# Performance work log

Measured on AMD Instinct MI355X. Metric: run time of the kernel, lower is better.

Reference implementation:

```python
import jax, jax.numpy as jnp
import numpy as np

TOP_K = 2  # config.n_expert_per_token


def setup_inputs() -> dict:
    key = jax.random.key(0)
    ks = jax.random.split(key, 5)
    B, T, C, E, F = 2, 2048, 2048, 8, 1024
    scale = 0.02
    return {
        "x": jax.random.normal(ks[0], (B, T, C), jnp.float32),
        "w_router": jax.random.normal(ks[1], (C, E), jnp.float32) * scale,
        "w1": jax.random.normal(ks[2], (E, C, F), jnp.float32) * scale,  # fc_1 (gate proj)
        "w3": jax.random.normal(ks[3], (E, C, F), jnp.float32) * scale,  # fc_2 (up proj)
        "w2": jax.random.normal(ks[4], (E, F, C), jnp.float32) * scale,  # proj (down)
    }


def reference(x, w_router, w1, w3, w2):
    B, T, C = x.shape
    xt = x.reshape(-1, C)                                  # [N, C]
    N = xt.shape[0]
    E = w_router.shape[1]
    # Router: topk logits, softmax over the selected k in fp32
    logits = xt @ w_router                                 # [N, E]
    top_vals, top_idx = jax.lax.top_k(logits, TOP_K)       # [N, k]
    probs = jax.nn.softmax(top_vals.astype(jnp.float32), axis=1).astype(xt.dtype)
    # Per-token per-expert combine weight (0 for unselected experts).
    # topk indices are distinct per token, so scatter-add == scatter-set.
    w = jnp.zeros((N, E), xt.dtype).at[jnp.arange(N)[:, None], top_idx].add(probs)  # [N, E]
    # Dense grouped SwiGLU expert MLPs; zero-weight tokens contribute nothing.
    g = jnp.einsum('nc,ecf->enf', xt, w1)                  # [E, N, F]
    u = jnp.einsum('nc,ecf->enf', xt, w3)                  # [E, N, F]
    h = jax.nn.silu(g) * u                                 # [E, N, F]
    outs = jnp.einsum('enf,efc->enc', h, w2)               # [E, N, C]
    y = jnp.einsum('enc,ne->nc', outs, w)                  # weighted combine
    return y.reshape(B, T, C)
```

## Files before the change

### kernel.cpp

```cpp
#include <hip/hip_runtime.h>
#include <hip/hip_bf16.h>
#include <stdint.h>

#define N_TOK 4096
#define CDIM 2048
#define EXP 8
#define FDIM 1024
#define LDSTRIDE 40

typedef __attribute__((ext_vector_type(4))) float f32x4;
typedef __attribute__((ext_vector_type(8))) short bf16x8;

__global__ __launch_bounds__(256) void transpose_to_bf16(
    const float* __restrict__ in, __hip_bfloat16* __restrict__ out, int R, int Cc) {
  __shared__ float tile[32][33];
  int e = blockIdx.z;
  const float* ip = in + (size_t)e * R * Cc;
  __hip_bfloat16* op = out + (size_t)e * R * Cc;
  int r0 = blockIdx.y * 32, c0 = blockIdx.x * 32;
  int tc = threadIdx.x & 31, tr = threadIdx.x >> 5;
#pragma unroll
  for (int i = 0; i < 4; i++) {
    int r = tr + i * 8;
    tile[r][tc] = ip[(size_t)(r0 + r) * Cc + c0 + tc];
  }
  __syncthreads();
#pragma unroll
  for (int i = 0; i < 4; i++) {
    int r = tr + i * 8;
    op[(size_t)(c0 + r) * R + r0 + tc] = __float2bfloat16(tile[tc][r]);
  }
}

__global__ __launch_bounds__(256) void router_kernel(
    const float* __restrict__ x, const float* __restrict__ wr,
    __hip_bfloat16* __restrict__ x_bf, int* __restrict__ counts,
    int* __restrict__ pair_expert, float* __restrict__ pair_prob) {
  int tok = blockIdx.x;
  const float* xr = x + (size_t)tok * CDIM;
  int t = threadIdx.x;
  float acc[EXP];
#pragma unroll
  for (int e = 0; e < EXP; e++) acc[e] = 0.f;
#pragma unroll
  for (int j = 0; j < 8; j++) {
    int c = j * 256 + t;
    float xv = xr[c];
    x_bf[(size_t)tok * CDIM + c] = __float2bfloat16(xv);
    const float4* wr4 = (const float4*)(wr + (size_t)c * EXP);
    float4 wa = wr4[0], wb = wr4[1];
    acc[0] += xv * wa.x; acc[1] += xv * wa.y; acc[2] += xv * wa.z; acc[3] += xv * wa.w;
    acc[4] += xv * wb.x; acc[5] += xv * wb.y; acc[6] += xv * wb.z; acc[7] += xv * wb.w;
  }
#pragma unroll
  for (int e = 0; e < EXP; e++) {
#pragma unroll
    for (int off = 32; off > 0; off >>= 1) acc[e] += __shfl_down(acc[e], off, 64);
  }
  __shared__ float wsum[4][EXP];
  int wid = t >> 6, lane = t & 63;
  if (lane == 0) {
#pragma unroll
    for (int e = 0; e < EXP; e++) wsum[wid][e] = acc[e];
  }
  __syncthreads();
  if (t == 0) {
    float lg[EXP];
#pragma unroll
    for (int e = 0; e < EXP; e++) lg[e] = wsum[0][e] + wsum[1][e] + wsum[2][e] + wsum[3][e];
    int i0 = 0;
#pragma unroll
    for (int e = 1; e < EXP; e++) if (lg[e] > lg[i0]) i0 = e;
    int i1 = (i0 == 0) ? 1 : 0;
#pragma unroll
    for (int e = 0; e < EXP; e++) if (e != i0 && lg[e] > lg[i1]) i1 = e;
    float e1 = __expf(lg[i1] - lg[i0]);
    float p0 = 1.f / (1.f + e1);
    pair_expert[tok * 2 + 0] = i0;
    pair_expert[tok * 2 + 1] = i1;
    pair_prob[tok * 2 + 0] = p0;
    pair_prob[tok * 2 + 1] = e1 * p0;
    atomicAdd(&counts[i0], 1);
    atomicAdd(&counts[i1], 1);
  }
}

__global__ void scan_kernel(const int* __restrict__ counts, int* __restrict__ bases) {
  if (threadIdx.x == 0) {
    int s = 0;
    for (int e = 0; e < EXP; e++) { bases[e] = s; s += counts[e]; }
  }
}

__global__ __launch_bounds__(256) void scatter_kernel(
    const int* __restrict__ pair_expert, const int* __restrict__ bases,
    int* __restrict__ cursors, int* __restrict__ lists) {
  int tok = blockIdx.x * 256 + threadIdx.x;
  if (tok >= N_TOK) return;
#pragma unroll
  for (int k = 0; k < 2; k++) {
    int e = pair_expert[tok * 2 + k];
    int pos = atomicAdd(&cursors[e], 1);
    lists[bases[e] + pos] = tok * 2 + k;
  }
}

__global__ __launch_bounds__(256) void gemm1_kernel(
    const __hip_bfloat16* __restrict__ xbf, const __hip_bfloat16* __restrict__ w1t,
    const __hip_bfloat16* __restrict__ w3t, const int* __restrict__ counts,
    const int* __restrict__ bases, const int* __restrict__ lists,
    __hip_bfloat16* __restrict__ h) {
  int e = blockIdx.z;
  int n_e = counts[e];
  int m0 = blockIdx.y * 128;
  if (m0 >= n_e) return;
  int base = bases[e];
  int f0 = blockIdx.x * 64;

  __shared__ short As[128 * LDSTRIDE];
  __shared__ short B1s[64 * LDSTRIDE];
  __shared__ short B3s[64 * LDSTRIDE];

  int t = threadIdx.x;
  int lane = t & 63, wid = t >> 6;
  int wm = (wid & 1) * 64, wf = (wid >> 1) * 32;

  int arow = t >> 1;
  int achunk = (t & 1) * 16;
  int rr = m0 + arow;
  int pair = lists[base + ((rr < n_e) ? rr : 0)];
  int tokA = pair >> 1;

  const short* xs = (const short*)xbf;
  const short* b1p = (const short*)(w1t) + (size_t)e * FDIM * CDIM;
  const short* b3p = (const short*)(w3t) + (size_t)e * FDIM * CDIM;
  int brow = (t & 127) >> 1;
  bool doB1 = (t < 128);
  const short* bsrc = doB1 ? b1p : b3p;
  short* bdst = doB1 ? B1s : B3s;

  f32x4 zero = {0.f, 0.f, 0.f, 0.f};
  f32x4 accg[4][2], accu[4][2];
#pragma unroll
  for (int i = 0; i < 4; i++)
#pragma unroll
    for (int j = 0; j < 2; j++) { accg[i][j] = zero; accu[i][j] = zero; }

  for (int kk = 0; kk < CDIM; kk += 32) {
    __syncthreads();
    {
      const int4* src = (const int4*)(xs + (size_t)tokA * CDIM + kk + achunk);
      int4* dst = (int4*)(As + arow * LDSTRIDE + achunk);
      dst[0] = src[0];
      dst[1] = src[1];
      const int4* src2 = (const int4*)(bsrc + (size_t)(f0 + brow) * CDIM + kk + achunk);
      int4* dst2 = (int4*)(bdst + brow * LDSTRIDE + achunk);
      dst2[0] = src2[0];
      dst2[1] = src2[1];
    }
    __syncthreads();
    int kq = (lane >> 4) * 8;
    int rsel = lane & 15;
    bf16x8 af[4], b1f[2], b3f[2];
#pragma unroll
    for (int i = 0; i < 4; i++)
      af[i] = *(const bf16x8*)(As + (wm + i * 16 + rsel) * LDSTRIDE + kq);
#pragma unroll
    for (int j = 0; j < 2; j++) {
      b1f[j] = *(const bf16x8*)(B1s + (wf + j * 16 + rsel) * LDSTRIDE + kq);
      b3f[j] = *(const bf16x8*)(B3s + (wf + j * 16 + rsel) * LDSTRIDE + kq);
    }
#pragma unroll
    for (int i = 0; i < 4; i++)
#pragma unroll
      for (int j = 0; j < 2; j++) {
        accg[i][j] = __builtin_amdgcn_mfma_f32_16x16x32_bf16(af[i], b1f[j], accg[i][j], 0, 0, 0);
        accu[i][j] = __builtin_amdgcn_mfma_f32_16x16x32_bf16(af[i], b3f[j], accu[i][j], 0, 0, 0);
      }
  }

  int col = lane & 15;
  int rbase = (lane >> 4) * 4;
#pragma unroll
  for (int i = 0; i < 4; i++) {
#pragma unroll
    for (int r = 0; r < 4; r++) {
      int m = m0 + wm + i * 16 + rbase + r;
      if (m < n_e) {
        size_t hrow = (size_t)(base + m) * FDIM;
#pragma unroll
        for (int j = 0; j < 2; j++) {
          int f = f0 + wf + j * 16 + col;
          float g = accg[i][j][r];
          float u = accu[i][j][r];
          float sg = g / (1.f + __expf(-g));
          h[hrow + f] = __float2bfloat16(sg * u);
        }
      }
    }
  }
}

__global__ __launch_bounds__(256) void gemm2_kernel(
    const __hip_bfloat16* __restrict__ h, const __hip_bfloat16* __restrict__ w2t,
    const int* __restrict__ counts, const int* __restrict__ bases,
    const int* __restrict__ lists, const float* __restrict__ pair_prob,
    float* __restrict__ out) {
  int e = blockIdx.z;
  int n_e = counts[e];
  int m0 = blockIdx.y * 128;
  if (m0 >= n_e) return;
  int base = bases[e];
  int c0 = blockIdx.x * 128;

  __shared__ short As[128 * LDSTRIDE];
  __shared__ short Bs[128 * LDSTRIDE];

  int t = threadIdx.x;
  int lane = t & 63, wid = t >> 6;
  int wm = (wid & 1) * 64, wn = (wid >> 1) * 64;

  int arow = t >> 1;
  int achunk = (t & 1) * 16;
  int hr = base + m0 + arow;
  if (hr > 2 * N_TOK - 1) hr = 2 * N_TOK - 1;
  const short* hp = (const short*)h;
  const short* bp = (const short*)(w2t) + (size_t)e * CDIM * FDIM;

  f32x4 zero = {0.f, 0.f, 0.f, 0.f};
  f32x4 acc[4][4];
#pragma unroll
  for (int i = 0; i < 4; i++)
#pragma unroll
    for (int j = 0; j < 4; j++) acc[i][j] = zero;

  for (int kk = 0; kk < FDIM; kk += 32) {
    __syncthreads();
    {
      const int4* src = (const int4*)(hp + (size_t)hr * FDIM + kk + achunk);
      int4* dst = (int4*)(As + arow * LDSTRIDE + achunk);
      dst[0] = src[0];
      dst[1] = src[1];
      const int4* src2 = (const int4*)(bp + (size_t)(c0 + arow) * FDIM + kk + achunk);
      int4* dst2 = (int4*)(Bs + arow * LDSTRIDE + achunk);
      dst2[0] = src2[0];
      dst2[1] = src2[1];
    }
    __syncthreads();
    int kq = (lane >> 4) * 8;
    int rsel = lane & 15;
    bf16x8 af[4], bfr[4];
#pragma unroll
    for (int i = 0; i < 4; i++)
      af[i] = *(const bf16x8*)(As + (wm + i * 16 + rsel) * LDSTRIDE + kq);
#pragma unroll
    for (int j = 0; j < 4; j++)
      bfr[j] = *(const bf16x8*)(Bs + (wn + j * 16 + rsel) * LDSTRIDE + kq);
#pragma unroll
    for (int i = 0; i < 4; i++)
#pragma unroll
      for (int j = 0; j < 4; j++)
        acc[i][j] = __builtin_amdgcn_mfma_f32_16x16x32_bf16(af[i], bfr[j], acc[i][j], 0, 0, 0);
  }

  int col = lane & 15;
  int rbase = (lane >> 4) * 4;
#pragma unroll
  for (int i = 0; i < 4; i++) {
#pragma unroll
    for (int r = 0; r < 4; r++) {
      int m = m0 + wm + i * 16 + rbase + r;
      if (m < n_e) {
        int pr = lists[base + m];
        int tok = pr >> 1;
        float p = pair_prob[pr];
        size_t orow = (size_t)tok * CDIM;
#pragma unroll
        for (int j = 0; j < 4; j++) {
          int c = c0 + wn + j * 16 + col;
          atomicAdd(&out[orow + c], acc[i][j][r] * p);
        }
      }
    }
  }
}

extern "C" void kernel_launch(void* const* d_in, const int* in_sizes, int n_in,
                              void* d_out, int out_size, void* d_ws, size_t ws_size,
                              hipStream_t stream) {
  const float* x  = (const float*)d_in[0];
  const float* wr = (const float*)d_in[1];
  const float* w1 = (const float*)d_in[2];
  const float* w3 = (const float*)d_in[3];
  const float* w2 = (const float*)d_in[4];
  float* out = (float*)d_out;

  char* ws = (char*)d_ws;
  __hip_bfloat16* x_bf = (__hip_bfloat16*)(ws);
  __hip_bfloat16* h    = (__hip_bfloat16*)(ws + 16777216);
  __hip_bfloat16* w1t  = (__hip_bfloat16*)(ws + 33554432);
  __hip_bfloat16* w3t  = (__hip_bfloat16*)(ws + 67108864);
  __hip_bfloat16* w2t  = (__hip_bfloat16*)(ws + 100663296);
  int* counts  = (int*)(ws + 134217728);
  int* bases   = counts + 8;
  int* cursors = counts + 16;
  int* pair_expert = (int*)(ws + 134217728 + 128);
  float* pair_prob = (float*)(ws + 134217728 + 128 + 32768);
  int* lists       = (int*)(ws + 134217728 + 128 + 65536);

  hipMemsetAsync(d_out, 0, (size_t)N_TOK * CDIM * sizeof(float), stream);
  hipMemsetAsync(counts, 0, 128, stream);

  transpose_to_bf16<<<dim3(FDIM / 32, CDIM / 32, EXP), 256, 0, stream>>>(w1, w1t, CDIM, FDIM);
  transpose_to_bf16<<<dim3(FDIM / 32, CDIM / 32, EXP), 256, 0, stream>>>(w3, w3t, CDIM, FDIM);
  transpose_to_bf16<<<dim3(CDIM / 32, FDIM / 32, EXP), 256, 0, stream>>>(w2, w2t, FDIM, CDIM);

  router_kernel<<<N_TOK, 256, 0, stream>>>(x, wr, x_bf, counts, pair_expert, pair_prob);
  scan_kernel<<<1, 64, 0, stream>>>(counts, bases);
  scatter_kernel<<<N_TOK / 256, 256, 0, stream>>>(pair_expert, bases, cursors, lists);

  gemm1_kernel<<<dim3(FDIM / 64, N_TOK / 128, EXP), 256, 0, stream>>>(
      x_bf, w1t, w3t, counts, bases, lists, h);
  gemm2_kernel<<<dim3(CDIM / 128, N_TOK / 128, EXP), 256, 0, stream>>>(
      h, w2t, counts, bases, lists, pair_prob, out);
}
```

Before: 632.2 us.

## Use direct global-to-LDS loads in expert GEMMs and vectorize weight transpose

Both expert GEMM kernels now stage A and B tiles with global_load_lds 16-byte transfers straight into LDS, which skips the register round trip. The LDS tiles are re-laid out into 16x32 fragment blocks so each lane reads its MFMA operand contiguously. The weight transpose kernel now uses float4 loads, 64-row tiles and 16-byte bf16 stores to cut transaction count. The new LDS layout has no padding, so fragment reads may hit bank conflicts, and the global reads per row become more scattered across lanes.

```diff
diff --git a/kernel.cpp b/kernel.cpp
--- a/kernel.cpp
+++ b/kernel.cpp
@@ -6,30 +6,40 @@
 #define CDIM 2048
 #define EXP 8
 #define FDIM 1024
-#define LDSTRIDE 40
 
 typedef __attribute__((ext_vector_type(4))) float f32x4;
 typedef __attribute__((ext_vector_type(8))) short bf16x8;
 
+__device__ __forceinline__ void g2l16(const void* g, void* l) {
+  __builtin_amdgcn_global_load_lds(
+      (const __attribute__((address_space(1))) void*)g,
+      (__attribute__((address_space(3))) void*)l, 16, 0, 0);
+}
+
 __global__ __launch_bounds__(256) void transpose_to_bf16(
     const float* __restrict__ in, __hip_bfloat16* __restrict__ out, int R, int Cc) {
-  __shared__ float tile[32][33];
+  __shared__ float tile[32][65];
   int e = blockIdx.z;
   const float* ip = in + (size_t)e * R * Cc;
   __hip_bfloat16* op = out + (size_t)e * R * Cc;
-  int r0 = blockIdx.y * 32, c0 = blockIdx.x * 32;
-  int tc = threadIdx.x & 31, tr = threadIdx.x >> 5;
-#pragma unroll
-  for (int i = 0; i < 4; i++) {
-    int r = tr + i * 8;
-    tile[r][tc] = ip[(size_t)(r0 + r) * Cc + c0 + tc];
+  int r0 = blockIdx.y * 64, c0 = blockIdx.x * 32;
+  int t = threadIdx.x;
+#pragma unroll
+  for (int p = 0; p < 2; p++) {
+    int f = t + p * 256;
+    int r = f >> 3, c4 = (f & 7) * 4;
+    float4 v = *(const float4*)(ip + (size_t)(r0 + r) * Cc + c0 + c4);
+    tile[c4 + 0][r] = v.x;
+    tile[c4 + 1][r] = v.y;
+    tile[c4 + 2][r] = v.z;
+    tile[c4 + 3][r] = v.w;
   }
   __syncthreads();
-#pragma unroll
-  for (int i = 0; i < 4; i++) {
-    int r = tr + i * 8;
-    op[(size_t)(c0 + r) * R + r0 + tc] = __float2bfloat16(tile[tc][r]);
-  }
+  int c = t >> 3, seg = (t & 7) * 8;
+  union { int4 v; __hip_bfloat16 h[8]; } u;
+#pragma unroll
+  for (int j = 0; j < 8; j++) u.h[j] = __float2bfloat16(tile[c][seg + j]);
+  *(int4*)(op + (size_t)(c0 + c) * R + r0 + seg) = u.v;
 }
 
 __global__ __launch_bounds__(256) void router_kernel(
@@ -117,27 +127,31 @@
   int base = bases[e];
   int f0 = blockIdx.x * 64;
 
-  __shared__ short As[128 * LDSTRIDE];
-  __shared__ short B1s[64 * LDSTRIDE];
-  __shared__ short B3s[64 * LDSTRIDE];
+  __shared__ alignas(16) short As[128 * 32];
+  __shared__ alignas(16) short B1s[64 * 32];
+  __shared__ alignas(16) short B3s[64 * 32];
 
   int t = threadIdx.x;
   int lane = t & 63, wid = t >> 6;
-  int wm = (wid & 1) * 64, wf = (wid >> 1) * 32;
-
-  int arow = t >> 1;
-  int achunk = (t & 1) * 16;
-  int rr = m0 + arow;
-  int pair = lists[base + ((rr < n_e) ? rr : 0)];
-  int tokA = pair >> 1;
+  int lr = lane & 15;
+  int lk = (lane >> 4) * 8;
 
   const short* xs = (const short*)xbf;
-  const short* b1p = (const short*)(w1t) + (size_t)e * FDIM * CDIM;
-  const short* b3p = (const short*)(w3t) + (size_t)e * FDIM * CDIM;
-  int brow = (t & 127) >> 1;
-  bool doB1 = (t < 128);
-  const short* bsrc = doB1 ? b1p : b3p;
-  short* bdst = doB1 ? B1s : B3s;
+  const short* b1p = (const short*)w1t + (size_t)e * FDIM * CDIM;
+  const short* b3p = (const short*)w3t + (size_t)e * FDIM * CDIM;
+
+  int r0a = m0 + (2 * wid) * 16 + lr;
+  int r1a = m0 + (2 * wid + 1) * 16 + lr;
+  int t0 = lists[base + ((r0a < n_e) ? r0a : (n_e - 1))] >> 1;
+  int t1 = lists[base + ((r1a < n_e) ? r1a : (n_e - 1))] >> 1;
+  const short* aptr0 = xs + (size_t)t0 * CDIM + lk;
+  const short* aptr1 = xs + (size_t)t1 * CDIM + lk;
+  const short* bptr1 = b1p + (size_t)(f0 + wid * 16 + lr) * CDIM + lk;
+  const short* bptr3 = b3p + (size_t)(f0 + wid * 16 + lr) * CDIM + lk;
+  short* ldsA0 = &As[(2 * wid) * 512];
+  short* ldsA1 = &As[(2 * wid + 1) * 512];
+  short* ldsB1 = &B1s[wid * 512];
+  short* ldsB3 = &B3s[wid * 512];
 
   f32x4 zero = {0.f, 0.f, 0.f, 0.f};
   f32x4 accg[4][2], accu[4][2];
@@ -146,29 +160,24 @@
 #pragma unroll
     for (int j = 0; j < 2; j++) { accg[i][j] = zero; accu[i][j] = zero; }
 
+  int asub = (wid & 1) * 4;
+  int bsub = (wid >> 1) * 2;
+
   for (int kk = 0; kk < CDIM; kk += 32) {
     __syncthreads();
-    {
-      const int4* src = (const int4*)(xs + (size_t)tokA * CDIM + kk + achunk);
-      int4* dst = (int4*)(As + arow * LDSTRIDE + achunk);
-      dst[0] = src[0];
-      dst[1] = src[1];
-      const int4* src2 = (const int4*)(bsrc + (size_t)(f0 + brow) * CDIM + kk + achunk);
-      int4* dst2 = (int4*)(bdst + brow * LDSTRIDE + achunk);
-      dst2[0] = src2[0];
-      dst2[1] = src2[1];
-    }
+    g2l16(aptr0 + kk, ldsA0);
+    g2l16(aptr1 + kk, ldsA1);
+    g2l16(bptr1 + kk, ldsB1);
+    g2l16(bptr3 + kk, ldsB3);
     __syncthreads();
-    int kq = (lane >> 4) * 8;
-    int rsel = lane & 15;
     bf16x8 af[4], b1f[2], b3f[2];
 #pragma unroll
     for (int i = 0; i < 4; i++)
-      af[i] = *(const bf16x8*)(As + (wm + i * 16 + rsel) * LDSTRIDE + kq);
+      af[i] = *(const bf16x8*)&As[(asub + i) * 512 + lane * 8];
 #pragma unroll
     for (int j = 0; j < 2; j++) {
-      b1f[j] = *(const bf16x8*)(B1s + (wf + j * 16 + rsel) * LDSTRIDE + kq);
-      b3f[j] = *(const bf16x8*)(B3s + (wf + j * 16 + rsel) * LDSTRIDE + kq);
+      b1f[j] = *(const bf16x8*)&B1s[(bsub + j) * 512 + lane * 8];
+      b3f[j] = *(const bf16x8*)&B3s[(bsub + j) * 512 + lane * 8];
     }
 #pragma unroll
     for (int i = 0; i < 4; i++)
@@ -179,6 +188,7 @@
       }
   }
 
+  int wm = (wid & 1) * 64, wf = (wid >> 1) * 32;
   int col = lane & 15;
   int rbase = (lane >> 4) * 4;
 #pragma unroll
@@ -213,19 +223,29 @@
   int base = bases[e];
   int c0 = blockIdx.x * 128;
 
-  __shared__ short As[128 * LDSTRIDE];
-  __shared__ short Bs[128 * LDSTRIDE];
+  __shared__ alignas(16) short As[128 * 32];
+  __shared__ alignas(16) short Bs[128 * 32];
 
   int t = threadIdx.x;
   int lane = t & 63, wid = t >> 6;
-  int wm = (wid & 1) * 64, wn = (wid >> 1) * 64;
-
-  int arow = t >> 1;
-  int achunk = (t & 1) * 16;
-  int hr = base + m0 + arow;
-  if (hr > 2 * N_TOK - 1) hr = 2 * N_TOK - 1;
+  int lr = lane & 15;
+  int lk = (lane >> 4) * 8;
+
   const short* hp = (const short*)h;
-  const short* bp = (const short*)(w2t) + (size_t)e * CDIM * FDIM;
+  const short* bp = (const short*)w2t + (size_t)e * CDIM * FDIM;
+
+  int hr0 = base + m0 + (2 * wid) * 16 + lr;
+  int hr1 = base + m0 + (2 * wid + 1) * 16 + lr;
+  if (hr0 > 2 * N_TOK - 1) hr0 = 2 * N_TOK - 1;
+  if (hr1 > 2 * N_TOK - 1) hr1 = 2 * N_TOK - 1;
+  const short* aptr0 = hp + (size_t)hr0 * FDIM + lk;
+  const short* aptr1 = hp + (size_t)hr1 * FDIM + lk;
+  const short* bptr0 = bp + (size_t)(c0 + (2 * wid) * 16 + lr) * FDIM + lk;
+  const short* bptr1 = bp + (size_t)(c0 + (2 * wid + 1) * 16 + lr) * FDIM + lk;
+  short* ldsA0 = &As[(2 * wid) * 512];
+  short* ldsA1 = &As[(2 * wid + 1) * 512];
+  short* ldsB0 = &Bs[(2 * wid) * 512];
+  short* ldsB1 = &Bs[(2 * wid + 1) * 512];
 
   f32x4 zero = {0.f, 0.f, 0.f, 0.f};
   f32x4 acc[4][4];
@@ -234,28 +254,23 @@
 #pragma unroll
     for (int j = 0; j < 4; j++) acc[i][j] = zero;
 
+  int asub = (wid & 1) * 4;
+  int bsub = (wid >> 1) * 4;
+
   for (int kk = 0; kk < FDIM; kk += 32) {
     __syncthreads();
-    {
-      const int4* src = (const int4*)(hp + (size_t)hr * FDIM + kk + achunk);
-      int4* dst = (int4*)(As + arow * LDSTRIDE + achunk);
-      dst[0] = src[0];
-      dst[1] = src[1];
-      const int4* src2 = (const int4*)(bp + (size_t)(c0 + arow) * FDIM + kk + achunk);
-      int4* dst2 = (int4*)(Bs + arow * LDSTRIDE + achunk);
-      dst2[0] = src2[0];
-      dst2[1] = src2[1];
-    }
+    g2l16(aptr0 + kk, ldsA0);
+    g2l16(aptr1 + kk, ldsA1);
+    g2l16(bptr0 + kk, ldsB0);
+    g2l16(bptr1 + kk, ldsB1);
     __syncthreads();
-    int kq = (lane >> 4) * 8;
-    int rsel = lane & 15;
     bf16x8 af[4], bfr[4];
 #pragma unroll
     for (int i = 0; i < 4; i++)
-      af[i] = *(const bf16x8*)(As + (wm + i * 16 + rsel) * LDSTRIDE + kq);
+      af[i] = *(const bf16x8*)&As[(asub + i) * 512 + lane * 8];
 #pragma unroll
     for (int j = 0; j < 4; j++)
-      bfr[j] = *(const bf16x8*)(Bs + (wn + j * 16 + rsel) * LDSTRIDE + kq);
+      bfr[j] = *(const bf16x8*)&Bs[(bsub + j) * 512 + lane * 8];
 #pragma unroll
     for (int i = 0; i < 4; i++)
 #pragma unroll
@@ -263,6 +278,7 @@
         acc[i][j] = __builtin_amdgcn_mfma_f32_16x16x32_bf16(af[i], bfr[j], acc[i][j], 0, 0, 0);
   }
 
+  int wm = (wid & 1) * 64, wn = (wid >> 1) * 64;
   int col = lane & 15;
   int rbase = (lane >> 4) * 4;
 #pragma unroll
@@ -311,9 +327,9 @@
   hipMemsetAsync(d_out, 0, (size_t)N_TOK * CDIM * sizeof(float), stream);
   hipMemsetAsync(counts, 0, 128, stream);
 
-  transpose_to_bf16<<<dim3(FDIM / 32, CDIM / 32, EXP), 256, 0, stream>>>(w1, w1t, CDIM, FDIM);
-  transpose_to_bf16<<<dim3(FDIM / 32, CDIM / 32, EXP), 256, 0, stream>>>(w3, w3t, CDIM, FDIM);
-  transpose_to_bf16<<<dim3(CDIM / 32, FDIM / 32, EXP), 256, 0, stream>>>(w2, w2t, FDIM, CDIM);
+  transpose_to_bf16<<<dim3(FDIM / 32, CDIM / 64, EXP), 256, 0, stream>>>(w1, w1t, CDIM, FDIM);
+  transpose_to_bf16<<<dim3(FDIM / 32, CDIM / 64, EXP), 256, 0, stream>>>(w3, w3t, CDIM, FDIM);
+  transpose_to_bf16<<<dim3(CDIM / 32, FDIM / 64, EXP), 256, 0, stream>>>(w2, w2t, FDIM, CDIM);
 
   router_kernel<<<N_TOK, 256, 0, stream>>>(x, wr, x_bf, counts, pair_expert, pair_prob);
   scan_kernel<<<1, 64, 0, stream>>>(counts, bases);
```

Result: slower. 688.6 us (+8.9%).

## Register-prefetch next K tile in MoE GEMMs and vectorize weight transpose

Applied to the files above, without the earlier changes.

Both grouped GEMM kernels now load the next K-slice from global memory into registers right after the barrier, so the fetch overlaps the MFMA work on the current LDS tile instead of stalling at the top of each iteration. The weight transpose-to-bf16 kernel moves to 64x64 tiles, reading with float4 and writing 16 bf16 values per thread as two int4 stores, which cuts the number of memory instructions. This costs extra live registers in the GEMMs, which may lower occupancy. The transpose's column-major LDS writes may also hit bank conflicts.

```diff
diff --git a/kernel.cpp b/kernel.cpp
--- a/kernel.cpp
+++ b/kernel.cpp
@@ -13,22 +13,33 @@
 
 __global__ __launch_bounds__(256) void transpose_to_bf16(
     const float* __restrict__ in, __hip_bfloat16* __restrict__ out, int R, int Cc) {
-  __shared__ float tile[32][33];
+  __shared__ float tile[64][65];
   int e = blockIdx.z;
   const float* ip = in + (size_t)e * R * Cc;
   __hip_bfloat16* op = out + (size_t)e * R * Cc;
-  int r0 = blockIdx.y * 32, c0 = blockIdx.x * 32;
-  int tc = threadIdx.x & 31, tr = threadIdx.x >> 5;
-#pragma unroll
-  for (int i = 0; i < 4; i++) {
-    int r = tr + i * 8;
-    tile[r][tc] = ip[(size_t)(r0 + r) * Cc + c0 + tc];
+  int r0 = blockIdx.y * 64, c0 = blockIdx.x * 64;
+  int t = threadIdx.x;
+  {
+    int r = t >> 2, cb = (t & 3) * 16;
+    const float* src = ip + (size_t)(r0 + r) * Cc + c0 + cb;
+#pragma unroll
+    for (int i = 0; i < 4; i++) {
+      float4 v = *(const float4*)(src + i * 4);
+      tile[cb + i * 4 + 0][r] = v.x;
+      tile[cb + i * 4 + 1][r] = v.y;
+      tile[cb + i * 4 + 2][r] = v.z;
+      tile[cb + i * 4 + 3][r] = v.w;
+    }
   }
   __syncthreads();
-#pragma unroll
-  for (int i = 0; i < 4; i++) {
-    int r = tr + i * 8;
-    op[(size_t)(c0 + r) * R + r0 + tc] = __float2bfloat16(tile[tc][r]);
+  {
+    int c = t >> 2, sb = (t & 3) * 16;
+    union { int4 v[2]; __hip_bfloat16 h[16]; } u;
+#pragma unroll
+    for (int j = 0; j < 16; j++) u.h[j] = __float2bfloat16(tile[c][sb + j]);
+    __hip_bfloat16* dst = op + (size_t)(c0 + c) * R + r0 + sb;
+    *(int4*)(dst) = u.v[0];
+    *(int4*)(dst + 8) = u.v[1];
   }
 }
 
@@ -123,7 +134,6 @@
 
   int t = threadIdx.x;
   int lane = t & 63, wid = t >> 6;
-  int wm = (wid & 1) * 64, wf = (wid >> 1) * 32;
 
   int arow = t >> 1;
   int achunk = (t & 1) * 16;
@@ -132,12 +142,19 @@
   int tokA = pair >> 1;
 
   const short* xs = (const short*)xbf;
-  const short* b1p = (const short*)(w1t) + (size_t)e * FDIM * CDIM;
-  const short* b3p = (const short*)(w3t) + (size_t)e * FDIM * CDIM;
+  const short* b1p = (const short*)w1t + (size_t)e * FDIM * CDIM;
+  const short* b3p = (const short*)w3t + (size_t)e * FDIM * CDIM;
   int brow = (t & 127) >> 1;
   bool doB1 = (t < 128);
-  const short* bsrc = doB1 ? b1p : b3p;
-  short* bdst = doB1 ? B1s : B3s;
+  const short* bsrc = (doB1 ? b1p : b3p) + (size_t)(f0 + brow) * CDIM + achunk;
+  short* bdst = (doB1 ? B1s : B3s) + brow * LDSTRIDE + achunk;
+  const short* asrc = xs + (size_t)tokA * CDIM + achunk;
+  short* adst = As + arow * LDSTRIDE + achunk;
+
+  int4 pa0 = *(const int4*)(asrc);
+  int4 pa1 = *(const int4*)(asrc + 8);
+  int4 pb0 = *(const int4*)(bsrc);
+  int4 pb1 = *(const int4*)(bsrc + 8);
 
   f32x4 zero = {0.f, 0.f, 0.f, 0.f};
   f32x4 accg[4][2], accu[4][2];
@@ -146,21 +163,23 @@
 #pragma unroll
     for (int j = 0; j < 2; j++) { accg[i][j] = zero; accu[i][j] = zero; }
 
+  int wm = (wid & 1) * 64, wf = (wid >> 1) * 32;
+  int kq = (lane >> 4) * 8;
+  int rsel = lane & 15;
+
   for (int kk = 0; kk < CDIM; kk += 32) {
     __syncthreads();
-    {
-      const int4* src = (const int4*)(xs + (size_t)tokA * CDIM + kk + achunk);
-      int4* dst = (int4*)(As + arow * LDSTRIDE + achunk);
-      dst[0] = src[0];
-      dst[1] = src[1];
-      const int4* src2 = (const int4*)(bsrc + (size_t)(f0 + brow) * CDIM + kk + achunk);
-      int4* dst2 = (int4*)(bdst + brow * LDSTRIDE + achunk);
-      dst2[0] = src2[0];
-      dst2[1] = src2[1];
-    }
+    *(int4*)(adst) = pa0;
+    *(int4*)(adst + 8) = pa1;
+    *(int4*)(bdst) = pb0;
+    *(int4*)(bdst + 8) = pb1;
     __syncthreads();
-    int kq = (lane >> 4) * 8;
-    int rsel = lane & 15;
+    if (kk + 32 < CDIM) {
+      pa0 = *(const int4*)(asrc + kk + 32);
+      pa1 = *(const int4*)(asrc + kk + 40);
+      pb0 = *(const int4*)(bsrc + kk + 32);
+      pb1 = *(const int4*)(bsrc + kk + 40);
+    }
     bf16x8 af[4], b1f[2], b3f[2];
 #pragma unroll
     for (int i = 0; i < 4; i++)
@@ -218,14 +237,22 @@
 
   int t = threadIdx.x;
   int lane = t & 63, wid = t >> 6;
-  int wm = (wid & 1) * 64, wn = (wid >> 1) * 64;
 
   int arow = t >> 1;
   int achunk = (t & 1) * 16;
   int hr = base + m0 + arow;
   if (hr > 2 * N_TOK - 1) hr = 2 * N_TOK - 1;
   const short* hp = (const short*)h;
-  const short* bp = (const short*)(w2t) + (size_t)e * CDIM * FDIM;
+  const short* bp = (const short*)w2t + (size_t)e * CDIM * FDIM;
+  const short* asrc = hp + (size_t)hr * FDIM + achunk;
+  const short* bsrc = bp + (size_t)(c0 + arow) * FDIM + achunk;
+  short* adst = As + arow * LDSTRIDE + achunk;
+  short* bdst = Bs + arow * LDSTRIDE + achunk;
+
+  int4 pa0 = *(const int4*)(asrc);
+  int4 pa1 = *(const int4*)(asrc + 8);
+  int4 pb0 = *(const int4*)(bsrc);
+  int4 pb1 = *(const int4*)(bsrc + 8);
 
   f32x4 zero = {0.f, 0.f, 0.f, 0.f};
   f32x4 acc[4][4];
@@ -234,21 +261,23 @@
 #pragma unroll
     for (int j = 0; j < 4; j++) acc[i][j] = zero;
 
+  int wm = (wid & 1) * 64, wn = (wid >> 1) * 64;
+  int kq = (lane >> 4) * 8;
+  int rsel = lane & 15;
+
   for (int kk = 0; kk < FDIM; kk += 32) {
     __syncthreads();
-    {
-      const int4* src = (const int4*)(hp + (size_t)hr * FDIM + kk + achunk);
-      int4* dst = (int4*)(As + arow * LDSTRIDE + achunk);
-      dst[0] = src[0];
-      dst[1] = src[1];
-      const int4* src2 = (const int4*)(bp + (size_t)(c0 + arow) * FDIM + kk + achunk);
-      int4* dst2 = (int4*)(Bs + arow * LDSTRIDE + achunk);
-      dst2[0] = src2[0];
-      dst2[1] = src2[1];
-    }
+    *(int4*)(adst) = pa0;
+    *(int4*)(adst + 8) = pa1;
+    *(int4*)(bdst) = pb0;
+    *(int4*)(bdst + 8) = pb1;
     __syncthreads();
-    int kq = (lane >> 4) * 8;
-    int rsel = lane & 15;
+    if (kk + 32 < FDIM) {
+      pa0 = *(const int4*)(asrc + kk + 32);
+      pa1 = *(const int4*)(asrc + kk + 40);
+      pb0 = *(const int4*)(bsrc + kk + 32);
+      pb1 = *(const int4*)(bsrc + kk + 40);
+    }
     bf16x8 af[4], bfr[4];
 #pragma unroll
     for (int i = 0; i < 4; i++)
@@ -311,9 +340,9 @@
   hipMemsetAsync(d_out, 0, (size_t)N_TOK * CDIM * sizeof(float), stream);
   hipMemsetAsync(counts, 0, 128, stream);
 
-  transpose_to_bf16<<<dim3(FDIM / 32, CDIM / 32, EXP), 256, 0, stream>>>(w1, w1t, CDIM, FDIM);
-  transpose_to_bf16<<<dim3(FDIM / 32, CDIM / 32, EXP), 256, 0, stream>>>(w3, w3t, CDIM, FDIM);
-  transpose_to_bf16<<<dim3(CDIM / 32, FDIM / 32, EXP), 256, 0, stream>>>(w2, w2t, FDIM, CDIM);
+  transpose_to_bf16<<<dim3(FDIM / 64, CDIM / 64, EXP), 256, 0, stream>>>(w1, w1t, CDIM, FDIM);
+  transpose_to_bf16<<<dim3(FDIM / 64, CDIM / 64, EXP), 256, 0, stream>>>(w3, w3t, CDIM, FDIM);
+  transpose_to_bf16<<<dim3(CDIM / 64, FDIM / 64, EXP), 256, 0, stream>>>(w2, w2t, FDIM, CDIM);
 
   router_kernel<<<N_TOK, 256, 0, stream>>>(x, wr, x_bf, counts, pair_expert, pair_prob);
   scan_kernel<<<1, 64, 0, stream>>>(counts, bases);
```

Measured after the change: 625.8 us. Within noise of the previous version (-1.0%).
